# Kernel optimization log

Measured on AMD Instinct MI355X. Metric: run time of the kernel, lower is better.

Reference implementation:

```python
import jax, jax.numpy as jnp
import numpy as np

N_FACTORS = 4
N_ITERATIONS = 2
N_LAYERS = 1
DEG_EPS = 1e-8
L2_EPS = 1e-12


def _l2norm(x):
    # torch F.normalize(p=2, dim=1): x / max(||x||, eps)
    n = jnp.sqrt(jnp.sum(x * x, axis=-1, keepdims=True))
    return x / jnp.maximum(n, L2_EPS)


def setup_inputs() -> dict:
    key = jax.random.key(0)
    k1, k2, k3, k4, k5, k6, k7 = jax.random.split(key, 7)
    n_users, n_items, D, M, B = 40000, 20000, 128, 600000, 4096
    return {
        "user_emb": jax.random.normal(k1, (n_users, D), dtype=jnp.float32) * 0.02,
        "item_emb": jax.random.normal(k2, (n_items, D), dtype=jnp.float32) * 0.02,
        "row": jax.random.randint(k3, (M,), 0, n_users, dtype=jnp.int32),
        "col": jax.random.randint(k4, (M,), 0, n_items, dtype=jnp.int32),
        "users": jax.random.randint(k5, (B,), 0, n_users, dtype=jnp.int32),
        "pos": jax.random.randint(k6, (B,), 0, n_items, dtype=jnp.int32),
        "neg": jax.random.randint(k7, (B,), 0, n_items, dtype=jnp.int32),
    }


def reference(user_emb, item_emb, row, col, users, pos, neg):
    n_users = user_emb.shape[0]
    n_nodes = n_users + item_emb.shape[0]
    D = user_emb.shape[1]
    d = D // N_FACTORS

    # symmetric edge list: (u -> i+offset) and (i+offset -> u)
    h = jnp.concatenate([row, col + n_users])  # [E]
    t = jnp.concatenate([col + n_users, row])  # [E]
    E = h.shape[0]

    ego = jnp.concatenate([user_emb, item_emb], axis=0)  # [N, D]
    A = jnp.ones((E, N_FACTORS), dtype=ego.dtype)
    all_emb = [ego]

    for _layer in range(N_LAYERS):
        ego_f = ego.reshape(n_nodes, N_FACTORS, d)  # factor chunks
        factor_emb = None
        for it in range(N_ITERATIONS):
            # build_matrix: per-factor edge softmax + D^-0.5 A D^-0.5
            norm_A = jax.nn.softmax(A, axis=1)                         # [E, F]
            deg = jax.ops.segment_sum(norm_A, h, num_segments=n_nodes)  # [N, F]
            deg = 1.0 / jnp.sqrt(jnp.maximum(deg, DEG_EPS))
            edge_w = norm_A * deg[h] * deg[t]                          # [E, F]
            # per-factor sparse spmm: gather tail, weight, scatter to head
            edge_val = ego_f[t] * edge_w[:, :, None]                   # [E, F, d]
            factor_emb = jax.ops.segment_sum(edge_val, h, num_segments=n_nodes)  # [N, F, d]
            if it < N_ITERATIONS - 1:
                # routing score update (final update is unused by forward)
                hn = _l2norm(factor_emb[h])   # [E, F, d]
                tn = _l2norm(ego_f[t])        # [E, F, d]
                A = A + jnp.sum(hn * jnp.tanh(tn), axis=-1)
        ego = factor_emb.reshape(n_nodes, D)
        all_emb.append(ego)

    out = jnp.mean(jnp.stack(all_emb, axis=1), axis=1)  # [N, D]
    u_g = out[:n_users]
    i_g = out[n_users:]
    return u_g[users], i_g[pos], i_g[neg]
```

## Files before the change

kernel.cpp:

```cpp
#include <hip/hip_runtime.h>
#include <hip/hip_fp16.h>
#include <math.h>

#define NU 40000
#define NI 20000
#define NN 60000
#define DD 128
#define NF 4
#define ME 600000
#define NE 1200000
#define NB 4096
#define NBLK 235
#define CPAD 16


__device__ __forceinline__ const float* node_row(const float* ue, const float* ie, int n) {
    return (n < NU) ? (ue + (size_t)n * DD) : (ie + (size_t)(n - NU) * DD);
}

typedef _Float16 hf2_t __attribute__((ext_vector_type(2)));
__device__ __forceinline__ float fdot2f(unsigned int a, unsigned int b, float c) {
#if __has_builtin(__builtin_amdgcn_fdot2)
    return __builtin_amdgcn_fdot2(__builtin_bit_cast(hf2_t, a),
                                  __builtin_bit_cast(hf2_t, b), c, false);
#else
    float2 fa = __half22float2(__builtin_bit_cast(__half2, a));
    float2 fb = __half22float2(__builtin_bit_cast(__half2, b));
    return c + fa.x * fb.x + fa.y * fb.y;
#endif
}


__global__ void k_zero(int* counts, unsigned char* flags) {
    int i = blockIdx.x * blockDim.x + threadIdx.x;
    if (i < NN * CPAD) counts[i] = 0;
    if (i < NN) flags[i] = 0;
}

__global__ void k_flag(const int* __restrict__ users, const int* __restrict__ pos,
                       const int* __restrict__ neg, unsigned char* __restrict__ flags) {
    int i = blockIdx.x * blockDim.x + threadIdx.x;
    if (i >= 3 * NB) return;
    int which = i >> 12, k = i & 4095;
    int n = (which == 0) ? users[k] : ((which == 1) ? NU + pos[k] : NU + neg[k]);
    flags[n] = 1;
}

__global__ void k_count(const int* __restrict__ row, const int* __restrict__ col,
                        int* __restrict__ counts, int* __restrict__ rank) {
    int base = (blockIdx.x * blockDim.x + threadIdx.x) * 4;
    if (base >= NE) return;
    int4 h4;
    if (base < ME) {
        h4 = *(const int4*)(row + base);
    } else {
        int4 c4 = *(const int4*)(col + (base - ME));
        h4 = make_int4(NU + c4.x, NU + c4.y, NU + c4.z, NU + c4.w);
    }
    int4 r;
    r.x = atomicAdd(&counts[h4.x * CPAD], 1);
    r.y = atomicAdd(&counts[h4.y * CPAD], 1);
    r.z = atomicAdd(&counts[h4.z * CPAD], 1);
    r.w = atomicAdd(&counts[h4.w * CPAD], 1);
    *(int4*)(rank + base) = r;
}


__global__ void k_scanA(const int* __restrict__ counts, int* __restrict__ pre,
                        int* __restrict__ bsum) {
    int tid = threadIdx.x;
    int i = blockIdx.x * 256 + tid;
    int v = (i < NN) ? counts[i * CPAD] : 0;
    int lane = tid & 63, w = tid >> 6;
    int s = v;
    #pragma unroll
    for (int off = 1; off < 64; off <<= 1) {
        int o = __shfl_up(s, off);
        if (lane >= off) s += o;
    }
    __shared__ int wsum[4];
    if (lane == 63) wsum[w] = s;
    __syncthreads();
    int add = 0;
    #pragma unroll
    for (int k = 0; k < 4; ++k) add += (k < w) ? wsum[k] : 0;
    if (i < NN) pre[i] = s - v + add;
    if (tid == 255) bsum[blockIdx.x] = add + s;
}

__global__ void k_scanB(const int* __restrict__ bsum, int* __restrict__ boff) {
    int tid = threadIdx.x;
    int v = (tid < NBLK) ? bsum[tid] : 0;
    int lane = tid & 63, w = tid >> 6;
    int s = v;
    #pragma unroll
    for (int off = 1; off < 64; off <<= 1) {
        int o = __shfl_up(s, off);
        if (lane >= off) s += o;
    }
    __shared__ int wsum[4];
    if (lane == 63) wsum[w] = s;
    __syncthreads();
    int add = 0;
    #pragma unroll
    for (int k = 0; k < 4; ++k) add += (k < w) ? wsum[k] : 0;
    if (tid < NBLK) boff[tid] = s - v + add;
}

__global__ void k_scanC(const int* __restrict__ pre, const int* __restrict__ boff,
                        const int* __restrict__ counts,
                        int* __restrict__ row_ptr, float* __restrict__ dinv0) {
    int i = blockIdx.x * 256 + threadIdx.x;
    if (i < NN) {
        row_ptr[i] = pre[i] + boff[blockIdx.x];
        dinv0[i]   = 1.0f / sqrtf(fmaxf(0.25f * (float)counts[i * CPAD], 1e-8f));
    }
    if (i == 0) row_ptr[NN] = NE;
}

__global__ void k_fill(const int* __restrict__ row, const int* __restrict__ col,
                       const int* __restrict__ row_ptr, const int* __restrict__ rank,
                       unsigned short* __restrict__ t_sorted) {
    int base = (blockIdx.x * blockDim.x + threadIdx.x) * 4;
    if (base >= NE) return;
    int4 h4, t4;
    if (base < ME) {
        h4 = *(const int4*)(row + base);
        int4 c4 = *(const int4*)(col + base);
        t4 = make_int4(NU + c4.x, NU + c4.y, NU + c4.z, NU + c4.w);
    } else {
        int4 c4 = *(const int4*)(col + (base - ME));
        h4 = make_int4(NU + c4.x, NU + c4.y, NU + c4.z, NU + c4.w);
        t4 = *(const int4*)(row + (base - ME));
    }
    int4 r = *(const int4*)(rank + base);
    t_sorted[row_ptr[h4.x] + r.x] = (unsigned short)t4.x;
    t_sorted[row_ptr[h4.y] + r.y] = (unsigned short)t4.y;
    t_sorted[row_ptr[h4.z] + r.z] = (unsigned short)t4.z;
    t_sorted[row_ptr[h4.w] + r.w] = (unsigned short)t4.w;
}

__global__ void k_prep(const float* __restrict__ ue, const float* __restrict__ ie,
                       const float* __restrict__ dinv0, __half* __restrict__ dst) {
    int i = blockIdx.x * blockDim.x + threadIdx.x;
    if (i >= NN * DD / 8) return;
    int n = i >> 4;
    int off = (i & 15) * 8;
    const float* src = node_row(ue, ie, n) + off;
    float w = dinv0[n];
    float4 a = *(const float4*)src;
    float4 b = *(const float4*)(src + 4);
    __half2 h[4] = { __floats2half2_rn(w * a.x, w * a.y), __floats2half2_rn(w * a.z, w * a.w),
                     __floats2half2_rn(w * b.x, w * b.y), __floats2half2_rn(w * b.z, w * b.w) };
    ((float4*)dst)[i] = *(float4*)h;
}

__global__ void k_prop0_norm(const float* __restrict__ ue, const float* __restrict__ ie,
                             const __half* __restrict__ ego16s,
                             const int* __restrict__ row_ptr,
                             const unsigned short* __restrict__ t_sorted,
                             __half* __restrict__ fnorm, __half* __restrict__ ttan) {
    int n = blockIdx.x * 8 + (threadIdx.x >> 5);
    if (n >= NN) return;
    int j = threadIdx.x & 31;
    int p0 = row_ptr[n], p1 = row_ptr[n + 1];
    float4 acc = make_float4(0.f, 0.f, 0.f, 0.f);
    #pragma unroll 8
    for (int p = p0; p < p1; ++p) {
        int t = t_sorted[p];
        float2 raw = ((const float2*)(ego16s + (size_t)t * DD))[j];
        float2 v01 = __half22float2(*(const __half2*)&raw.x);
        float2 v23 = __half22float2(*(const __half2*)&raw.y);
        acc.x += v01.x; acc.y += v01.y;
        acc.z += v23.x; acc.w += v23.y;
    }
    float ss = acc.x * acc.x + acc.y * acc.y + acc.z * acc.z + acc.w * acc.w;
    ss += __shfl_xor(ss, 1); ss += __shfl_xor(ss, 2); ss += __shfl_xor(ss, 4);
    float inv = 1.0f / fmaxf(sqrtf(ss), 1e-12f);
    __half2 f01 = __floats2half2_rn(acc.x * inv, acc.y * inv);
    __half2 f23 = __floats2half2_rn(acc.z * inv, acc.w * inv);
    __half2 fpair[2] = { f01, f23 };
    ((float2*)(fnorm + (size_t)n * DD))[j] = *(float2*)fpair;

    float4 u = ((const float4*)node_row(ue, ie, n))[j];
    float s2 = u.x * u.x + u.y * u.y + u.z * u.z + u.w * u.w;
    s2 += __shfl_xor(s2, 1); s2 += __shfl_xor(s2, 2); s2 += __shfl_xor(s2, 4);
    float inv2 = 1.0f / fmaxf(sqrtf(s2), 1e-12f);
    __half2 t01 = __floats2half2_rn(tanhf(u.x * inv2), tanhf(u.y * inv2));
    __half2 t23 = __floats2half2_rn(tanhf(u.z * inv2), tanhf(u.w * inv2));
    __half2 tpair[2] = { t01, t23 };
    ((float2*)(ttan + (size_t)n * DD))[j] = *(float2*)tpair;
}

__global__ void k_attn_deg(const int* __restrict__ row_ptr,
                           const unsigned short* __restrict__ t_sorted,
                           const __half* __restrict__ fnorm, const __half* __restrict__ ttan,
                           const unsigned char* __restrict__ flags,
                           float* __restrict__ normA, float* __restrict__ dinv1) {
    int n = blockIdx.x * 4 + (threadIdx.x >> 6);
    if (n >= NN) return;
    int lane = threadIdx.x & 63;
    int g  = lane >> 4;
    int il = lane & 15;
    int f  = il >> 2;
    int p0 = row_ptr[n], p1 = row_ptr[n + 1];
    bool writeA = flags[n] != 0;
    uint4 au = ((const uint4*)(fnorm + (size_t)n * DD))[il];
    float dacc = 0.0f;
    #pragma unroll 4
    for (int pb = p0; pb < p1; pb += 4) {
        int p = pb + g;
        bool valid = p < p1;
        int pc = valid ? p : (p1 - 1);
        int t = t_sorted[pc];
        uint4 bu = ((const uint4*)(ttan + (size_t)t * DD))[il];
        float s = 0.0f;
        s = fdot2f(au.x, bu.x, s);
        s = fdot2f(au.y, bu.y, s);
        s = fdot2f(au.z, bu.z, s);
        s = fdot2f(au.w, bu.w, s);
        s += __shfl_xor(s, 1);
        s += __shfl_xor(s, 2);
        float m1 = fmaxf(s, __shfl_xor(s, 4));
        float mx = fmaxf(m1, __shfl_xor(m1, 8));
        float e = __expf(s - mx);
        float sum = e;
        sum += __shfl_xor(sum, 4);
        sum += __shfl_xor(sum, 8);
        float v = e * __builtin_amdgcn_rcpf(sum);
        if (valid) {
            if (writeA && (il & 3) == 0) normA[(size_t)pc * 4 + f] = v;
            dacc += v;
        }
    }
    dacc += __shfl_xor(dacc, 16);
    dacc += __shfl_xor(dacc, 32);
    if (g == 0 && (il & 3) == 0)
        dinv1[(size_t)n * 4 + f] = 1.0f / sqrtf(fmaxf(dacc, 1e-8f));
}

__global__ void k_prop1_out(const float* __restrict__ ue, const float* __restrict__ ie,
                            const int* __restrict__ row_ptr,
                            const unsigned short* __restrict__ t_sorted,
                            const float* __restrict__ normA, const float* __restrict__ dinv1,
                            const int* __restrict__ users, const int* __restrict__ pos,
                            const int* __restrict__ neg, float* __restrict__ out) {
    int r = blockIdx.x * 8 + (threadIdx.x >> 5);
    if (r >= 3 * NB) return;
    int j = threadIdx.x & 31;
    int f = j >> 3;
    int which = r >> 12;
    int i = r & 4095;
    int n;
    if (which == 0)      n = users[i];
    else if (which == 1) n = NU + pos[i];
    else                 n = NU + neg[i];
    int p0 = row_ptr[n], p1 = row_ptr[n + 1];
    float4 acc = make_float4(0.f, 0.f, 0.f, 0.f);
    #pragma unroll 4
    for (int p = p0; p < p1; ++p) {
        int t = t_sorted[p];
        float w = normA[(size_t)p * 4 + f] * dinv1[(size_t)t * 4 + f];
        float4 v = ((const float4*)node_row(ue, ie, t))[j];
        acc.x += w * v.x; acc.y += w * v.y;
        acc.z += w * v.z; acc.w += w * v.w;
    }
    float dn = dinv1[(size_t)n * 4 + f];
    float4 e0 = ((const float4*)node_row(ue, ie, n))[j];
    ((float4*)(out + (size_t)r * DD))[j] =
        make_float4(0.5f * (e0.x + dn * acc.x), 0.5f * (e0.y + dn * acc.y),
                    0.5f * (e0.z + dn * acc.z), 0.5f * (e0.w + dn * acc.w));
}


extern "C" void kernel_launch(void* const* d_in, const int* in_sizes, int n_in,
                              void* d_out, int out_size, void* d_ws, size_t ws_size,
                              hipStream_t stream) {
    const float* ue   = (const float*)d_in[0];
    const float* ie   = (const float*)d_in[1];
    const int* row    = (const int*)d_in[2];
    const int* col    = (const int*)d_in[3];
    const int* users  = (const int*)d_in[4];
    const int* pos    = (const int*)d_in[5];
    const int* neg    = (const int*)d_in[6];
    float* out        = (float*)d_out;

    char* ws = (char*)d_ws;
    size_t off = 0;
    auto take = [&](size_t bytes) { void* p = ws + off; off += (bytes + 255) & ~(size_t)255; return p; };
    __half* fnorm    = (__half*)take((size_t)NN * DD * 2);
    __half* ttan     = (__half*)take((size_t)NN * DD * 2);
    __half* ego16s   = (__half*)take((size_t)NN * DD * 2);
    float*  normA    = (float*)take((size_t)NE * 4 * 4);
    float*  dinv1    = (float*)take((size_t)NN * 4 * 4);
    float*  dinv0    = (float*)take((size_t)NN * 4);
    int*    row_ptr  = (int*)take((size_t)(NN + 1) * 4);
    int*    counts   = (int*)take((size_t)NN * CPAD * 4);
    int*    pre      = (int*)take((size_t)NN * 4);
    int*    bsum     = (int*)take((size_t)NBLK * 4);
    int*    boff     = (int*)take((size_t)NBLK * 4);
    int*    rank     = (int*)take((size_t)NE * 4);
    unsigned short* t_sorted = (unsigned short*)take((size_t)NE * 2);
    unsigned char*  flags    = (unsigned char*)take((size_t)NN);
    if (off > ws_size) return;

    k_zero <<<(NN * CPAD + 255) / 256, 256, 0, stream>>>(counts, flags);
    k_flag <<<(3 * NB + 255) / 256, 256, 0, stream>>>(users, pos, neg, flags);
    k_count<<<(NE / 4 + 255) / 256, 256, 0, stream>>>(row, col, counts, rank);
    k_scanA<<<NBLK, 256, 0, stream>>>(counts, pre, bsum);
    k_scanB<<<1, 256, 0, stream>>>(bsum, boff);
    k_scanC<<<NBLK, 256, 0, stream>>>(pre, boff, counts, row_ptr, dinv0);
    k_prep <<<(NN * DD / 8 + 255) / 256, 256, 0, stream>>>(ue, ie, dinv0, ego16s);
    k_fill <<<(NE / 4 + 255) / 256, 256, 0, stream>>>(row, col, row_ptr, rank, t_sorted);
    k_prop0_norm<<<(NN + 7) / 8, 256, 0, stream>>>(ue, ie, ego16s, row_ptr, t_sorted,
                                                   fnorm, ttan);
    k_attn_deg<<<(NN + 3) / 4, 256, 0, stream>>>(row_ptr, t_sorted, fnorm, ttan,
                                                 flags, normA, (float*)dinv1);
    k_prop1_out<<<(3 * NB) / 8, 256, 0, stream>>>(ue, ie, row_ptr, t_sorted,
                                                  normA, (const float*)dinv1,
                                                  users, pos, neg, out);
}
```

Baseline: 286.0 us.

## Fuse first propagation into attention kernel and move tanh-norm into prep

Merges the first propagation (gather-sum plus L2 normalise) into the attention/degree kernel. The normalised factor row now stays in registers and is redistributed with shuffles instead of being written to and reread from a global fnorm buffer. The tanh of the normalised ego embedding moves into k_prep, which already loads each row, so it no longer needs a separate reload. The gather loop now uses 64-lane wavefronts covering two edges per step, at the cost of masking the tail edge and an extra cross-half reduction.

```diff
diff --git a/kernel.cpp b/kernel.cpp
--- a/kernel.cpp
+++ b/kernel.cpp
@@ -141,71 +141,75 @@
 }
 
 __global__ void k_prep(const float* __restrict__ ue, const float* __restrict__ ie,
-                       const float* __restrict__ dinv0, __half* __restrict__ dst) {
+                       const float* __restrict__ dinv0,
+                       __half* __restrict__ ego16s, __half* __restrict__ ttan) {
     int i = blockIdx.x * blockDim.x + threadIdx.x;
-    if (i >= NN * DD / 8) return;
+    if (i >= NN * 16) return;
     int n = i >> 4;
-    int off = (i & 15) * 8;
-    const float* src = node_row(ue, ie, n) + off;
-    float w = dinv0[n];
+    int il = i & 15;
+    const float* src = node_row(ue, ie, n) + il * 8;
     float4 a = *(const float4*)src;
     float4 b = *(const float4*)(src + 4);
+    float w = dinv0[n];
     __half2 h[4] = { __floats2half2_rn(w * a.x, w * a.y), __floats2half2_rn(w * a.z, w * a.w),
                      __floats2half2_rn(w * b.x, w * b.y), __floats2half2_rn(w * b.z, w * b.w) };
-    ((float4*)dst)[i] = *(float4*)h;
-}
-
-__global__ void k_prop0_norm(const float* __restrict__ ue, const float* __restrict__ ie,
-                             const __half* __restrict__ ego16s,
-                             const int* __restrict__ row_ptr,
-                             const unsigned short* __restrict__ t_sorted,
-                             __half* __restrict__ fnorm, __half* __restrict__ ttan) {
-    int n = blockIdx.x * 8 + (threadIdx.x >> 5);
+    ((float4*)ego16s)[i] = *(float4*)h;
+    float s2 = a.x * a.x + a.y * a.y + a.z * a.z + a.w * a.w
+             + b.x * b.x + b.y * b.y + b.z * b.z + b.w * b.w;
+    s2 += __shfl_xor(s2, 1); s2 += __shfl_xor(s2, 2);
+    float inv = 1.0f / fmaxf(sqrtf(s2), 1e-12f);
+    __half2 t[4] = { __floats2half2_rn(tanhf(a.x * inv), tanhf(a.y * inv)),
+                     __floats2half2_rn(tanhf(a.z * inv), tanhf(a.w * inv)),
+                     __floats2half2_rn(tanhf(b.x * inv), tanhf(b.y * inv)),
+                     __floats2half2_rn(tanhf(b.z * inv), tanhf(b.w * inv)) };
+    ((float4*)ttan)[i] = *(float4*)t;
+}
+
+__global__ void k_mega(const int* __restrict__ row_ptr,
+                       const unsigned short* __restrict__ t_sorted,
+                       const __half* __restrict__ ego16s, const __half* __restrict__ ttan,
+                       const unsigned char* __restrict__ flags,
+                       float* __restrict__ normA, float* __restrict__ dinv1) {
+    int n = blockIdx.x * 4 + (threadIdx.x >> 6);
     if (n >= NN) return;
-    int j = threadIdx.x & 31;
+    int lane = threadIdx.x & 63;
     int p0 = row_ptr[n], p1 = row_ptr[n + 1];
+    bool writeA = flags[n] != 0;
+
+    int g2 = lane >> 5;
+    int jl = lane & 31;
     float4 acc = make_float4(0.f, 0.f, 0.f, 0.f);
-    #pragma unroll 8
-    for (int p = p0; p < p1; ++p) {
-        int t = t_sorted[p];
-        float2 raw = ((const float2*)(ego16s + (size_t)t * DD))[j];
+    #pragma unroll 4
+    for (int pb = p0; pb < p1; pb += 2) {
+        int p = pb + g2;
+        bool valid = p < p1;
+        int pc = valid ? p : (p1 - 1);
+        float m = valid ? 1.0f : 0.0f;
+        int t = t_sorted[pc];
+        float2 raw = ((const float2*)(ego16s + (size_t)t * DD))[jl];
         float2 v01 = __half22float2(*(const __half2*)&raw.x);
         float2 v23 = __half22float2(*(const __half2*)&raw.y);
-        acc.x += v01.x; acc.y += v01.y;
-        acc.z += v23.x; acc.w += v23.y;
-    }
+        acc.x += m * v01.x; acc.y += m * v01.y;
+        acc.z += m * v23.x; acc.w += m * v23.y;
+    }
+    acc.x += __shfl_xor(acc.x, 32); acc.y += __shfl_xor(acc.y, 32);
+    acc.z += __shfl_xor(acc.z, 32); acc.w += __shfl_xor(acc.w, 32);
     float ss = acc.x * acc.x + acc.y * acc.y + acc.z * acc.z + acc.w * acc.w;
     ss += __shfl_xor(ss, 1); ss += __shfl_xor(ss, 2); ss += __shfl_xor(ss, 4);
     float inv = 1.0f / fmaxf(sqrtf(ss), 1e-12f);
-    __half2 f01 = __floats2half2_rn(acc.x * inv, acc.y * inv);
-    __half2 f23 = __floats2half2_rn(acc.z * inv, acc.w * inv);
-    __half2 fpair[2] = { f01, f23 };
-    ((float2*)(fnorm + (size_t)n * DD))[j] = *(float2*)fpair;
-
-    float4 u = ((const float4*)node_row(ue, ie, n))[j];
-    float s2 = u.x * u.x + u.y * u.y + u.z * u.z + u.w * u.w;
-    s2 += __shfl_xor(s2, 1); s2 += __shfl_xor(s2, 2); s2 += __shfl_xor(s2, 4);
-    float inv2 = 1.0f / fmaxf(sqrtf(s2), 1e-12f);
-    __half2 t01 = __floats2half2_rn(tanhf(u.x * inv2), tanhf(u.y * inv2));
-    __half2 t23 = __floats2half2_rn(tanhf(u.z * inv2), tanhf(u.w * inv2));
-    __half2 tpair[2] = { t01, t23 };
-    ((float2*)(ttan + (size_t)n * DD))[j] = *(float2*)tpair;
-}
-
-__global__ void k_attn_deg(const int* __restrict__ row_ptr,
-                           const unsigned short* __restrict__ t_sorted,
-                           const __half* __restrict__ fnorm, const __half* __restrict__ ttan,
-                           const unsigned char* __restrict__ flags,
-                           float* __restrict__ normA, float* __restrict__ dinv1) {
-    int n = blockIdx.x * 4 + (threadIdx.x >> 6);
-    if (n >= NN) return;
-    int lane = threadIdx.x & 63;
-    int g  = lane >> 4;
+    unsigned int u01 = __builtin_bit_cast(unsigned int,
+                         __floats2half2_rn(acc.x * inv, acc.y * inv));
+    unsigned int u23 = __builtin_bit_cast(unsigned int,
+                         __floats2half2_rn(acc.z * inv, acc.w * inv));
     int il = lane & 15;
-    int f  = il >> 2;
-    int p0 = row_ptr[n], p1 = row_ptr[n + 1];
-    bool writeA = flags[n] != 0;
-    uint4 au = ((const uint4*)(fnorm + (size_t)n * DD))[il];
+    uint4 au;
+    au.x = __shfl(u01, 2 * il);
+    au.y = __shfl(u23, 2 * il);
+    au.z = __shfl(u01, 2 * il + 1);
+    au.w = __shfl(u23, 2 * il + 1);
+
+    int g = lane >> 4;
+    int f = il >> 2;
     float dacc = 0.0f;
     #pragma unroll 4
     for (int pb = p0; pb < p1; pb += 4) {
@@ -288,7 +292,6 @@
     char* ws = (char*)d_ws;
     size_t off = 0;
     auto take = [&](size_t bytes) { void* p = ws + off; off += (bytes + 255) & ~(size_t)255; return p; };
-    __half* fnorm    = (__half*)take((size_t)NN * DD * 2);
     __half* ttan     = (__half*)take((size_t)NN * DD * 2);
     __half* ego16s   = (__half*)take((size_t)NN * DD * 2);
     float*  normA    = (float*)take((size_t)NE * 4 * 4);
@@ -310,12 +313,10 @@
     k_scanA<<<NBLK, 256, 0, stream>>>(counts, pre, bsum);
     k_scanB<<<1, 256, 0, stream>>>(bsum, boff);
     k_scanC<<<NBLK, 256, 0, stream>>>(pre, boff, counts, row_ptr, dinv0);
-    k_prep <<<(NN * DD / 8 + 255) / 256, 256, 0, stream>>>(ue, ie, dinv0, ego16s);
+    k_prep <<<(NN * 16 + 255) / 256, 256, 0, stream>>>(ue, ie, dinv0, ego16s, ttan);
     k_fill <<<(NE / 4 + 255) / 256, 256, 0, stream>>>(row, col, row_ptr, rank, t_sorted);
-    k_prop0_norm<<<(NN + 7) / 8, 256, 0, stream>>>(ue, ie, ego16s, row_ptr, t_sorted,
-                                                   fnorm, ttan);
-    k_attn_deg<<<(NN + 3) / 4, 256, 0, stream>>>(row_ptr, t_sorted, fnorm, ttan,
-                                                 flags, normA, (float*)dinv1);
+    k_mega <<<(NN + 3) / 4, 256, 0, stream>>>(row_ptr, t_sorted, ego16s, ttan,
+                                              flags, normA, (float*)dinv1);
     k_prop1_out<<<(3 * NB) / 8, 256, 0, stream>>>(ue, ie, row_ptr, t_sorted,
                                                   normA, (const float*)dinv1,
                                                   users, pos, neg, out);
```

Measured after the change: 277.4 us. 3.0% less time.
